# Kernel optimization log

Hardware: AMD Instinct MI355X
Metric: run time of the kernel (lower is better)

Reference implementation:

```python
import jax, jax.numpy as jnp
import numpy as np

N = 100000       # nodes
E = 3200000      # edges (before self loops)
EMB = 16         # embedding dim (EMB_SIZE)
H = 32           # hidden_size
NUM_EMB = 141
EDGE_DIM = 1     # NUM_EDGE_FEATURES
NEG_SLOPE = 0.2  # PyG GATConv default negative_slope


def setup_inputs() -> dict:
    key = jax.random.key(0)
    ks = jax.random.split(key, 18)
    f32 = jnp.float32
    return {
        "x_idx": jax.random.randint(ks[0], (N, 1), 0, NUM_EMB),
        "edge_index": jax.random.randint(ks[1], (2, E), 0, N),
        "edge_attr": jax.random.normal(ks[2], (E, EDGE_DIM), f32),
        # learned params
        "emb": jax.random.normal(ks[3], (NUM_EMB, EMB), f32) * 0.1,
        # conv1 (GATConv 16->32, heads=1, edge_dim=1)
        "W1": jax.random.normal(ks[4], (EMB, H), f32) * (1.0 / np.sqrt(EMB)),
        "as1": jax.random.normal(ks[5], (H,), f32) * 0.1,
        "ad1": jax.random.normal(ks[6], (H,), f32) * 0.1,
        "We1": jax.random.normal(ks[7], (EDGE_DIM, H), f32),
        "ae1": jax.random.normal(ks[8], (H,), f32) * 0.1,
        "b1": jnp.zeros((H,), f32),
        # conv2 (GATConv 32->32)
        "W2": jax.random.normal(ks[9], (H, H), f32) * (1.0 / np.sqrt(H)),
        "as2": jax.random.normal(ks[10], (H,), f32) * 0.1,
        "ad2": jax.random.normal(ks[11], (H,), f32) * 0.1,
        "We2": jax.random.normal(ks[12], (EDGE_DIM, H), f32),
        "ae2": jax.random.normal(ks[13], (H,), f32) * 0.1,
        "b2": jnp.zeros((H,), f32),
        # linear head 32->1
        "Wl": jax.random.normal(ks[14], (H, 1), f32) * (1.0 / np.sqrt(H)),
        "bl": jnp.zeros((1,), f32),
    }


def _add_self_loops(src, dst, ea):
    # PyG add_self_loops with fill_value='mean': loop edge_attr is the
    # segment-mean of incoming edge_attr per destination node.
    sums = jax.ops.segment_sum(ea, dst, num_segments=N)            # [N, EDGE_DIM]
    cnts = jax.ops.segment_sum(jnp.ones((ea.shape[0],), ea.dtype), dst, num_segments=N)
    loop_attr = sums / jnp.maximum(cnts, 1.0)[:, None]
    loop = jnp.arange(N, dtype=src.dtype)
    return (jnp.concatenate([src, loop]),
            jnp.concatenate([dst, loop]),
            jnp.concatenate([ea, loop_attr], axis=0))


def _gat_conv(x, src, dst, ea, W, a_s, a_d, We, a_e, b):
    h = x @ W                                   # [N, H]
    e = ea @ We                                 # [E2, H]
    alpha = jax.nn.leaky_relu((h @ a_s)[src] + (h @ a_d)[dst] + e @ a_e, NEG_SLOPE)
    # segment softmax over incoming edges of each dst node
    amax = jax.ops.segment_max(alpha, dst, num_segments=N)
    ex = jnp.exp(alpha - amax[dst])
    denom = jax.ops.segment_sum(ex, dst, num_segments=N)
    coef = ex / (denom[dst] + 1e-16)            # [E2]
    out = jax.ops.segment_sum(h[src] * coef[:, None], dst, num_segments=N)
    return out + b


def reference(x_idx, edge_index, edge_attr, emb, W1, as1, ad1, We1, ae1, b1,
              W2, as2, ad2, We2, ae2, b2, Wl, bl):
    src, dst, ea = _add_self_loops(edge_index[0], edge_index[1], edge_attr)
    x = emb[x_idx[:, 0]]                        # [N, EMB]
    x = _gat_conv(x, src, dst, ea, W1, as1, ad1, We1, ae1, b1)
    x = jax.nn.relu(x)                          # dropout is identity in eval mode
    x = _gat_conv(x, src, dst, ea, W2, as2, ad2, We2, ae2, b2)
    return x @ Wl + bl                          # [N, 1]
```

## Files before the change

### kernel.cpp

```cpp
#include <hip/hip_runtime.h>
#include <utility>

#define NN 100000
#define NE 3200000
#define H 32
#define EMBD 16
#define NEMB 141
#define NEG_SLOPE 0.2f
#define CSH 7
#define CN 128
#define NCO 782
#define CAP 4608
#define LCAP 4608
#define KCH 12800
#define GA 250

__device__ __forceinline__ float bf2f(unsigned short u) {
    return __int_as_float((int)u << 16);
}

template<class F, int... Is>
__device__ __forceinline__ void static_for_impl(F f, std::integer_sequence<int, Is...>) {
    (f(std::integral_constant<int, Is>{}), ...);
}
template<int N, class F>
__device__ __forceinline__ void static_for(F f) {
    static_for_impl(f, std::make_integer_sequence<int, N>{});
}

__global__ void k_tab(const float* __restrict__ emb, const float* __restrict__ W1,
                      const float* __restrict__ as1, const float* __restrict__ ad1,
                      const float* We1, const float* ae1,
                      const float* We2, const float* ae2,
                      const float* W2, const float* as2, const float* ad2,
                      const float* Wl, const float* b2, const float* bl,
                      float* tabH, float* tabS, float* tabD, float* scal,
                      float* was2, float* wad2, float* wl2, float* c0,
                      int* bcnt) {
    int gid = blockIdx.x * 64 + threadIdx.x;
    if (gid < NCO) bcnt[gid] = 0;
    int r = blockIdx.x, j = threadIdx.x;
    if (j >= 32) {
        if (r == 0 && j == 32) {
            float c1 = 0.f, c2 = 0.f;
            for (int k = 0; k < H; k++) {
                c1 += We1[k] * ae1[k];
                c2 += We2[k] * ae2[k];
            }
            scal[0] = c1; scal[1] = c2;
        }
        if (r == 1) {
            int k = j - 32;
            float s = 0.f, d = 0.f, l = 0.f;
            for (int q = 0; q < H; q++) {
                float w = W2[k * H + q];
                s += w * as2[q];
                d += w * ad2[q];
                l += w * Wl[q];
            }
            was2[k] = s; wad2[k] = d; wl2[k] = l;
        }
        if (r == 2 && j == 32) {
            float c = bl[0];
            for (int q = 0; q < H; q++) c += b2[q] * Wl[q];
            c0[0] = c;
        }
        return;
    }
    float acc = 0.f;
    #pragma unroll
    for (int k = 0; k < EMBD; k++) acc += emb[r * EMBD + k] * W1[k * H + j];
    tabH[r * H + j] = acc;
    float s = acc * as1[j];
    float d = acc * ad1[j];
    #pragma unroll
    for (int off = 16; off > 0; off >>= 1) {
        s += __shfl_down(s, off, 32);
        d += __shfl_down(d, off, 32);
    }
    if (j == 0) { tabS[r] = s; tabD[r] = d; }
}

__global__ __launch_bounds__(1024) void k_pscat(
                        const int* __restrict__ src, const int* __restrict__ dst,
                        const float* __restrict__ ea, const int* __restrict__ x_idx,
                        int* bcnt, long long* epk) {
    __shared__ long long st[KCH];
    __shared__ unsigned short cbuk[KCH];
    __shared__ int hist[NCO];
    __shared__ int scanb[1024];
    __shared__ int bas[NCO];
    __shared__ int allow[NCO];
    int t = threadIdx.x;
    int e0 = blockIdx.x * KCH;
    const int4*   d4 = (const int4*)(dst + e0);
    const int4*   s4 = (const int4*)(src + e0);
    const float4* a4 = (const float4*)(ea + e0);
    if (t < NCO) hist[t] = 0;
    __syncthreads();

    long long pkr[4][4];
    int       pcr[4][4];
    #pragma unroll
    for (int g = 0; g < 4; g++) {
        bool v = (g < 3) || (t < 128);
        if (v) {
            int gi = g * 1024 + t;
            int4 d = d4[gi];
            int4 s = s4[gi];
            float4 a = a4[gi];
            int x0 = x_idx[s.x], x1 = x_idx[s.y], x2 = x_idx[s.z], x3 = x_idx[s.w];
            int c0 = d.x >> CSH, c1 = d.y >> CSH, c2 = d.z >> CSH, c3 = d.w >> CSH;
            pkr[g][0] = ((long long)(unsigned)__float_as_int(a.x) << 32)
                      | (unsigned)(s.x | ((d.x & (CN - 1)) << 17) | (x0 << 24));
            pkr[g][1] = ((long long)(unsigned)__float_as_int(a.y) << 32)
                      | (unsigned)(s.y | ((d.y & (CN - 1)) << 17) | (x1 << 24));
            pkr[g][2] = ((long long)(unsigned)__float_as_int(a.z) << 32)
                      | (unsigned)(s.z | ((d.z & (CN - 1)) << 17) | (x2 << 24));
            pkr[g][3] = ((long long)(unsigned)__float_as_int(a.w) << 32)
                      | (unsigned)(s.w | ((d.w & (CN - 1)) << 17) | (x3 << 24));
            pcr[g][0] = (c0 << 14) | atomicAdd(&hist[c0], 1);
            pcr[g][1] = (c1 << 14) | atomicAdd(&hist[c1], 1);
            pcr[g][2] = (c2 << 14) | atomicAdd(&hist[c2], 1);
            pcr[g][3] = (c3 << 14) | atomicAdd(&hist[c3], 1);
        }
    }
    __syncthreads();

    int hv = (t < NCO) ? hist[t] : 0;
    scanb[t] = hv;
    __syncthreads();
    for (int s = 1; s < 1024; s <<= 1) {
        int x = (t >= s) ? scanb[t - s] : 0;
        __syncthreads();
        scanb[t] += x;
        __syncthreads();
    }
    scanb[t] -= hv;
    if (t < NCO) {
        if (hv) {
            int b = atomicAdd(&bcnt[t], hv);
            bas[t]   = t * CAP + b;
            allow[t] = CAP - b;
        } else {
            bas[t] = t * CAP; allow[t] = 0;
        }
    }
    __syncthreads();

    #pragma unroll
    for (int g = 0; g < 4; g++) {
        bool v = (g < 3) || (t < 128);
        if (v) {
            #pragma unroll
            for (int e = 0; e < 4; e++) {
                int c = pcr[g][e] >> 14;
                int r = pcr[g][e] & 0x3fff;
                int pos = scanb[c] + r;
                st[pos] = pkr[g][e];
                cbuk[pos] = (unsigned short)c;
            }
        }
    }
    __syncthreads();

    for (int i = t; i < KCH; i += 1024) {
        int c = cbuk[i];
        int l = i - scanb[c];
        if (l < allow[c]) epk[bas[c] + l] = st[i];
    }
}

__global__ void k_psort(const int* __restrict__ bcnt, long long* epk, int2* nfo) {
    __shared__ long long st[LCAP];
    __shared__ unsigned short rnk[LCAP];
    __shared__ int hist[CN], lofs[CN];
    int c = blockIdx.x, t = threadIdx.x;
    int base = c * CAP;
    int cnt = bcnt[c];
    if (cnt > CAP) cnt = CAP;
    if (t < CN) hist[t] = 0;
    __syncthreads();
    for (int k = t; k < cnt; k += 512) {
        long long pk = epk[base + k];
        st[k] = pk;
        rnk[k] = (unsigned short)atomicAdd(&hist[((int)pk >> 17) & (CN - 1)], 1);
    }
    __syncthreads();
    if (t < CN) lofs[t] = hist[t];
    __syncthreads();
    for (int s = 1; s < CN; s <<= 1) {
        int x = (t >= s && t < CN) ? lofs[t - s] : 0;
        __syncthreads();
        if (t < CN) lofs[t] += x;
        __syncthreads();
    }
    if (t < CN) {
        int ex = lofs[t] - hist[t];
        lofs[t] = ex;
        int node = c * CN + t;
        if (node < NN) nfo[node] = make_int2(base + ex, hist[t]);
    }
    __syncthreads();
    for (int k = t; k < cnt; k += 512) {
        long long pk = st[k];
        int ln = ((int)pk >> 17) & (CN - 1);
        epk[base + lofs[ln] + rnk[k]] = pk;
    }
}

__global__ void k_agg1(const int2* __restrict__ nfo, const long long* __restrict__ epk,
                       const float* __restrict__ tabS, const float* __restrict__ tabD,
                       const float* __restrict__ scal,
                       const float* __restrict__ tabH,
                       const int* __restrict__ xi,
                       const float* __restrict__ bias,
                       const float* __restrict__ was2, const float* __restrict__ wad2,
                       const float* __restrict__ wl2,
                       float2* __restrict__ g2, float* __restrict__ hd2) {
    int ln   = threadIdx.x & 7;
    int node = (blockIdx.x * blockDim.x + threadIdx.x) >> 3;
    if (node >= NN) return;
    int2 fo = nfo[node];
    int beg = fo.x;
    int dg  = fo.y;
    int end = beg + dg;
    float sc = scal[0];
    int xin = xi[node];
    float hdi = tabD[xin];

    float suma = 0.f, denp = 0.f;
    float4 acc = make_float4(0.f, 0.f, 0.f, 0.f);
    int base = beg;
    for (; end - base > 16; base += 32) {
        int pw[4] = {0, 0, 0, 0};
        #pragma unroll
        for (int e = 0; e < 4; e++) {
            int kk = base + 4 * ln + e;
            if (kk < end) {
                long long pk = epk[kk];
                int lo = (int)pk;
                float a = __int_as_float((int)(pk >> 32));
                suma += a;
                float hsv = tabS[(lo >> 24) & 0xff];
                float al = hsv + hdi + sc * a;
                al = (al > 0.f) ? al : NEG_SLOPE * al;
                int eb = __float_as_int(__expf(al));
                pw[e] = ((eb + 0x80) & 0xffffff00) | ((lo >> 24) & 0xff);
                denp += __int_as_float(pw[e] & 0xffffff00);
            }
        }
        static_for<32>([&](auto tc) {
            constexpr int t = decltype(tc)::value;
            int p = __builtin_amdgcn_ds_swizzle(pw[t & 3], ((t >> 2) << 5) | 0x18);
            float ext = __int_as_float(p & 0xffffff00);
            const float4 hv = *(const float4*)(tabH + ((p & 0xff) << 5) + (ln << 2));
            acc.x += ext * hv.x;
            acc.y += ext * hv.y;
            acc.z += ext * hv.z;
            acc.w += ext * hv.w;
        });
    }
    if (base < end) {
        int pw[2] = {0, 0};
        #pragma unroll
        for (int e = 0; e < 2; e++) {
            int kk = base + 2 * ln + e;
            if (kk < end) {
                long long pk = epk[kk];
                int lo = (int)pk;
                float a = __int_as_float((int)(pk >> 32));
                suma += a;
                float hsv = tabS[(lo >> 24) & 0xff];
                float al = hsv + hdi + sc * a;
                al = (al > 0.f) ? al : NEG_SLOPE * al;
                int eb = __float_as_int(__expf(al));
                pw[e] = ((eb + 0x80) & 0xffffff00) | ((lo >> 24) & 0xff);
                denp += __int_as_float(pw[e] & 0xffffff00);
            }
        }
        static_for<16>([&](auto tc) {
            constexpr int t = decltype(tc)::value;
            int p = __builtin_amdgcn_ds_swizzle(pw[t & 1], ((t >> 1) << 5) | 0x18);
            float ext = __int_as_float(p & 0xffffff00);
            const float4 hv = *(const float4*)(tabH + ((p & 0xff) << 5) + (ln << 2));
            acc.x += ext * hv.x;
            acc.y += ext * hv.y;
            acc.z += ext * hv.z;
            acc.w += ext * hv.w;
        });
    }
    #pragma unroll
    for (int o = 4; o > 0; o >>= 1) {
        suma += __shfl_xor(suma, o, 8);
        denp += __shfl_xor(denp, o, 8);
    }
    float la = suma / (float)((dg > 0) ? dg : 1);
    float alself = tabS[xin] + hdi + sc * la;
    alself = (alself > 0.f) ? alself : NEG_SLOPE * alself;
    float exs = __expf(alself);
    const float4 hvs = *(const float4*)(tabH + (xin << 5) + (ln << 2));
    acc.x += exs * hvs.x;
    acc.y += exs * hvs.y;
    acc.z += exs * hvs.z;
    acc.w += exs * hvs.w;
    float den = denp + exs + 1e-16f;

    const float4 b4 = *(const float4*)(bias + (ln << 2));
    float4 x;
    x.x = fmaxf(acc.x / den + b4.x, 0.f);
    x.y = fmaxf(acc.y / den + b4.y, 0.f);
    x.z = fmaxf(acc.z / den + b4.z, 0.f);
    x.w = fmaxf(acc.w / den + b4.w, 0.f);
    const float4 wa = *(const float4*)(was2 + (ln << 2));
    const float4 wd = *(const float4*)(wad2 + (ln << 2));
    const float4 wy = *(const float4*)(wl2  + (ln << 2));
    float sp = x.x * wa.x + x.y * wa.y + x.z * wa.z + x.w * wa.w;
    float dp = x.x * wd.x + x.y * wd.y + x.z * wd.z + x.w * wd.w;
    float yp = x.x * wy.x + x.y * wy.y + x.z * wy.z + x.w * wy.w;
    #pragma unroll
    for (int o = 4; o > 0; o >>= 1) {
        sp += __shfl_xor(sp, o, 8);
        dp += __shfl_xor(dp, o, 8);
        yp += __shfl_xor(yp, o, 8);
    }
    if (ln == 0) { g2[node] = make_float2(sp, yp); hd2[node] = dp; }
}

__global__ void k_agg2(const int2* __restrict__ nfo, const long long* __restrict__ epk,
                       const float2* __restrict__ g2, const float* __restrict__ hd2,
                       const float* __restrict__ scal, const float* __restrict__ c0p,
                       float* __restrict__ outF) {
    int lane = threadIdx.x & 31;
    int node = (blockIdx.x * blockDim.x + threadIdx.x) >> 5;
    if (node >= NN) return;
    int2 fo = nfo[node];
    int beg = fo.x;
    int dg  = fo.y;
    int end = beg + dg;
    float sc = scal[1];
    float hdi = hd2[node];
    float2 gn = g2[node];

    float num = 0.f, den = 0.f, suma = 0.f;
    for (int base = beg; base < end; base += 32) {
        int kk = base + lane;
        if (kk < end) {
            long long pk = epk[kk];
            float a = __int_as_float((int)(pk >> 32));
            int s = (int)pk & 0x1ffff;
            float2 g = g2[s];
            suma += a;
            float al = g.x + hdi + sc * a;
            al = (al > 0.f) ? al : NEG_SLOPE * al;
            float ex = __expf(al);
            num += ex * g.y;
            den += ex;
        }
    }
    #pragma unroll
    for (int o = 16; o > 0; o >>= 1) {
        num  += __shfl_xor(num, o, 32);
        den  += __shfl_xor(den, o, 32);
        suma += __shfl_xor(suma, o, 32);
    }
    float la = suma / (float)((dg > 0) ? dg : 1);
    float als = gn.x + hdi + sc * la;
    als = (als > 0.f) ? als : NEG_SLOPE * als;
    float exs = __expf(als);
    num += exs * gn.y;
    den += exs + 1e-16f;
    if (lane == 0) outF[node] = num / den + c0p[0];
}

extern "C" void kernel_launch(void* const* d_in, const int* in_sizes, int n_in,
                              void* d_out, int out_size, void* d_ws, size_t ws_size,
                              hipStream_t stream) {
    const int*   x_idx = (const int*)d_in[0];
    const int*   src   = (const int*)d_in[1];
    const int*   dst   = src + NE;
    const float* ea    = (const float*)d_in[2];
    const float* emb = (const float*)d_in[3];
    const float* W1  = (const float*)d_in[4];
    const float* as1 = (const float*)d_in[5];
    const float* ad1 = (const float*)d_in[6];
    const float* We1 = (const float*)d_in[7];
    const float* ae1 = (const float*)d_in[8];
    const float* b1  = (const float*)d_in[9];
    const float* W2  = (const float*)d_in[10];
    const float* as2 = (const float*)d_in[11];
    const float* ad2 = (const float*)d_in[12];
    const float* We2 = (const float*)d_in[13];
    const float* ae2 = (const float*)d_in[14];
    const float* b2  = (const float*)d_in[15];
    const float* Wl  = (const float*)d_in[16];
    const float* bl  = (const float*)d_in[17];
    float* out = (float*)d_out;

    float* ws   = (float*)d_ws;
    float* scal = ws;
    float* tabS = ws + 8;
    float* tabD = ws + 256;
    float* tabH = ws + 512;
    int*   bcnt = (int*)(ws + 5120);
    float* was2 = ws + 6144;
    float* wad2 = ws + 6208;
    float* wl2  = ws + 6272;
    float* c0   = ws + 6336;
    int2*  nfo = (int2*)(ws + 208192);
    float2* g2 = (float2*)(ws + 408192);
    long long* epk = (long long*)(ws + 2008192);
    float* hd2 = ws + 9315104;

    const int B = 256;
    int g1 = (NN * 8 + B - 1) / B;
    int g2g = (NN * H + B - 1) / B;

    k_tab<<<NEMB, 64, 0, stream>>>(emb, W1, as1, ad1, We1, ae1, We2, ae2,
                                   W2, as2, ad2, Wl, b2, bl,
                                   tabH, tabS, tabD, scal,
                                   was2, wad2, wl2, c0, bcnt);
    k_pscat<<<GA, 1024, 0, stream>>>(src, dst, ea, x_idx, bcnt, epk);
    k_psort<<<NCO, 512, 0, stream>>>(bcnt, epk, nfo);
    k_agg1<<<g1, B, 0, stream>>>(nfo, epk, tabS, tabD, scal, tabH,
                                 x_idx, b1, was2, wad2, wl2, g2, hd2);
    k_agg2<<<g2g, B, 0, stream>>>(nfo, epk, g2, hd2, scal, c0, out);
}
```

Baseline: 214.8 us.

## Fuse per-chunk node sort into both aggregation kernels via shared memory

```diff
diff --git a/kernel.cpp b/kernel.cpp
--- a/kernel.cpp
+++ b/kernel.cpp
@@ -14,10 +14,6 @@
 #define LCAP 4608
 #define KCH 12800
 #define GA 250
-
-__device__ __forceinline__ float bf2f(unsigned short u) {
-    return __int_as_float((int)u << 16);
-}
 
 template<class F, int... Is>
 __device__ __forceinline__ void static_for_impl(F f, std::integer_sequence<int, Is...>) {
@@ -171,45 +167,8 @@
     }
 }
 
-__global__ void k_psort(const int* __restrict__ bcnt, long long* epk, int2* nfo) {
-    __shared__ long long st[LCAP];
-    __shared__ unsigned short rnk[LCAP];
-    __shared__ int hist[CN], lofs[CN];
-    int c = blockIdx.x, t = threadIdx.x;
-    int base = c * CAP;
-    int cnt = bcnt[c];
-    if (cnt > CAP) cnt = CAP;
-    if (t < CN) hist[t] = 0;
-    __syncthreads();
-    for (int k = t; k < cnt; k += 512) {
-        long long pk = epk[base + k];
-        st[k] = pk;
-        rnk[k] = (unsigned short)atomicAdd(&hist[((int)pk >> 17) & (CN - 1)], 1);
-    }
-    __syncthreads();
-    if (t < CN) lofs[t] = hist[t];
-    __syncthreads();
-    for (int s = 1; s < CN; s <<= 1) {
-        int x = (t >= s && t < CN) ? lofs[t - s] : 0;
-        __syncthreads();
-        if (t < CN) lofs[t] += x;
-        __syncthreads();
-    }
-    if (t < CN) {
-        int ex = lofs[t] - hist[t];
-        lofs[t] = ex;
-        int node = c * CN + t;
-        if (node < NN) nfo[node] = make_int2(base + ex, hist[t]);
-    }
-    __syncthreads();
-    for (int k = t; k < cnt; k += 512) {
-        long long pk = st[k];
-        int ln = ((int)pk >> 17) & (CN - 1);
-        epk[base + lofs[ln] + rnk[k]] = pk;
-    }
-}
-
-__global__ void k_agg1(const int2* __restrict__ nfo, const long long* __restrict__ epk,
+__global__ __launch_bounds__(1024) void k_bagg1(
+                       const int* __restrict__ bcnt, const long long* __restrict__ epk,
                        const float* __restrict__ tabS, const float* __restrict__ tabD,
                        const float* __restrict__ scal,
                        const float* __restrict__ tabH,
@@ -218,12 +177,47 @@
                        const float* __restrict__ was2, const float* __restrict__ wad2,
                        const float* __restrict__ wl2,
                        float2* __restrict__ g2, float* __restrict__ hd2) {
-    int ln   = threadIdx.x & 7;
-    int node = (blockIdx.x * blockDim.x + threadIdx.x) >> 3;
+    __shared__ long long st[LCAP];
+    __shared__ int hist[CN], lofs[CN];
+    int c = blockIdx.x, t = threadIdx.x;
+    int wbase = c * CAP;
+    int cnt = bcnt[c];
+    if (cnt > CAP) cnt = CAP;
+    if (t < CN) hist[t] = 0;
+    __syncthreads();
+
+    long long pk0 = 0, pk1 = 0, pk2 = 0, pk3 = 0, pk4 = 0;
+    int rk0 = 0, rk1 = 0, rk2 = 0, rk3 = 0, rk4 = 0;
+    #define LDRK(J) { int k = (J) * 1024 + t; if (k < cnt) { \
+        pk##J = epk[wbase + k]; \
+        rk##J = atomicAdd(&hist[((int)pk##J >> 17) & (CN - 1)], 1); } }
+    LDRK(0) LDRK(1) LDRK(2) LDRK(3) LDRK(4)
+    #undef LDRK
+    __syncthreads();
+
+    if (t < CN) lofs[t] = hist[t];
+    __syncthreads();
+    for (int s = 1; s < CN; s <<= 1) {
+        int x = (t >= s && t < CN) ? lofs[t - s] : 0;
+        __syncthreads();
+        if (t < CN) lofs[t] += x;
+        __syncthreads();
+    }
+    if (t < CN) lofs[t] -= hist[t];
+    __syncthreads();
+
+    #define SCT(J) { int k = (J) * 1024 + t; if (k < cnt) \
+        st[lofs[((int)pk##J >> 17) & (CN - 1)] + rk##J] = pk##J; }
+    SCT(0) SCT(1) SCT(2) SCT(3) SCT(4)
+    #undef SCT
+    __syncthreads();
+
+    int ln   = t & 7;
+    int nl   = t >> 3;
+    int node = c * CN + nl;
     if (node >= NN) return;
-    int2 fo = nfo[node];
-    int beg = fo.x;
-    int dg  = fo.y;
+    int beg = lofs[nl];
+    int dg  = hist[nl];
     int end = beg + dg;
     float sc = scal[0];
     int xin = xi[node];
@@ -231,14 +225,14 @@
 
     float suma = 0.f, denp = 0.f;
     float4 acc = make_float4(0.f, 0.f, 0.f, 0.f);
-    int base = beg;
-    for (; end - base > 16; base += 32) {
+    int bse = beg;
+    for (; end - bse > 16; bse += 32) {
         int pw[4] = {0, 0, 0, 0};
         #pragma unroll
         for (int e = 0; e < 4; e++) {
-            int kk = base + 4 * ln + e;
+            int kk = bse + 4 * ln + e;
             if (kk < end) {
-                long long pk = epk[kk];
+                long long pk = st[kk];
                 int lo = (int)pk;
                 float a = __int_as_float((int)(pk >> 32));
                 suma += a;
@@ -251,8 +245,8 @@
             }
         }
         static_for<32>([&](auto tc) {
-            constexpr int t = decltype(tc)::value;
-            int p = __builtin_amdgcn_ds_swizzle(pw[t & 3], ((t >> 2) << 5) | 0x18);
+            constexpr int tt = decltype(tc)::value;
+            int p = __builtin_amdgcn_ds_swizzle(pw[tt & 3], ((tt >> 2) << 5) | 0x18);
             float ext = __int_as_float(p & 0xffffff00);
             const float4 hv = *(const float4*)(tabH + ((p & 0xff) << 5) + (ln << 2));
             acc.x += ext * hv.x;
@@ -261,13 +255,13 @@
             acc.w += ext * hv.w;
         });
     }
-    if (base < end) {
+    if (bse < end) {
         int pw[2] = {0, 0};
         #pragma unroll
         for (int e = 0; e < 2; e++) {
-            int kk = base + 2 * ln + e;
+            int kk = bse + 2 * ln + e;
             if (kk < end) {
-                long long pk = epk[kk];
+                long long pk = st[kk];
                 int lo = (int)pk;
                 float a = __int_as_float((int)(pk >> 32));
                 suma += a;
@@ -280,8 +274,8 @@
             }
         }
         static_for<16>([&](auto tc) {
-            constexpr int t = decltype(tc)::value;
-            int p = __builtin_amdgcn_ds_swizzle(pw[t & 1], ((t >> 1) << 5) | 0x18);
+            constexpr int tt = decltype(tc)::value;
+            int p = __builtin_amdgcn_ds_swizzle(pw[tt & 1], ((tt >> 1) << 5) | 0x18);
             float ext = __int_as_float(p & 0xffffff00);
             const float4 hv = *(const float4*)(tabH + ((p & 0xff) << 5) + (ln << 2));
             acc.x += ext * hv.x;
@@ -327,42 +321,75 @@
     if (ln == 0) { g2[node] = make_float2(sp, yp); hd2[node] = dp; }
 }
 
-__global__ void k_agg2(const int2* __restrict__ nfo, const long long* __restrict__ epk,
+__global__ __launch_bounds__(1024) void k_bagg2(
+                       const int* __restrict__ bcnt, const long long* __restrict__ epk,
                        const float2* __restrict__ g2, const float* __restrict__ hd2,
                        const float* __restrict__ scal, const float* __restrict__ c0p,
                        float* __restrict__ outF) {
-    int lane = threadIdx.x & 31;
-    int node = (blockIdx.x * blockDim.x + threadIdx.x) >> 5;
+    __shared__ long long st[LCAP];
+    __shared__ int hist[CN], lofs[CN];
+    int c = blockIdx.x, t = threadIdx.x;
+    int wbase = c * CAP;
+    int cnt = bcnt[c];
+    if (cnt > CAP) cnt = CAP;
+    if (t < CN) hist[t] = 0;
+    __syncthreads();
+
+    long long pk0 = 0, pk1 = 0, pk2 = 0, pk3 = 0, pk4 = 0;
+    int rk0 = 0, rk1 = 0, rk2 = 0, rk3 = 0, rk4 = 0;
+    #define LDRK(J) { int k = (J) * 1024 + t; if (k < cnt) { \
+        pk##J = epk[wbase + k]; \
+        rk##J = atomicAdd(&hist[((int)pk##J >> 17) & (CN - 1)], 1); } }
+    LDRK(0) LDRK(1) LDRK(2) LDRK(3) LDRK(4)
+    #undef LDRK
+    __syncthreads();
+
+    if (t < CN) lofs[t] = hist[t];
+    __syncthreads();
+    for (int s = 1; s < CN; s <<= 1) {
+        int x = (t >= s && t < CN) ? lofs[t - s] : 0;
+        __syncthreads();
+        if (t < CN) lofs[t] += x;
+        __syncthreads();
+    }
+    if (t < CN) lofs[t] -= hist[t];
+    __syncthreads();
+
+    #define SCT(J) { int k = (J) * 1024 + t; if (k < cnt) \
+        st[lofs[((int)pk##J >> 17) & (CN - 1)] + rk##J] = pk##J; }
+    SCT(0) SCT(1) SCT(2) SCT(3) SCT(4)
+    #undef SCT
+    __syncthreads();
+
+    int ln   = t & 7;
+    int nl   = t >> 3;
+    int node = c * CN + nl;
     if (node >= NN) return;
-    int2 fo = nfo[node];
-    int beg = fo.x;
-    int dg  = fo.y;
+    int beg = lofs[nl];
+    int dg  = hist[nl];
     int end = beg + dg;
     float sc = scal[1];
     float hdi = hd2[node];
     float2 gn = g2[node];
 
     float num = 0.f, den = 0.f, suma = 0.f;
-    for (int base = beg; base < end; base += 32) {
-        int kk = base + lane;
-        if (kk < end) {
-            long long pk = epk[kk];
-            float a = __int_as_float((int)(pk >> 32));
-            int s = (int)pk & 0x1ffff;
-            float2 g = g2[s];
-            suma += a;
-            float al = g.x + hdi + sc * a;
-            al = (al > 0.f) ? al : NEG_SLOPE * al;
-            float ex = __expf(al);
-            num += ex * g.y;
-            den += ex;
-        }
-    }
-    #pragma unroll
-    for (int o = 16; o > 0; o >>= 1) {
-        num  += __shfl_xor(num, o, 32);
-        den  += __shfl_xor(den, o, 32);
-        suma += __shfl_xor(suma, o, 32);
+    for (int kk = beg + ln; kk < end; kk += 8) {
+        long long pk = st[kk];
+        float a = __int_as_float((int)(pk >> 32));
+        int s = (int)pk & 0x1ffff;
+        float2 g = g2[s];
+        suma += a;
+        float al = g.x + hdi + sc * a;
+        al = (al > 0.f) ? al : NEG_SLOPE * al;
+        float ex = __expf(al);
+        num += ex * g.y;
+        den += ex;
+    }
+    #pragma unroll
+    for (int o = 4; o > 0; o >>= 1) {
+        num  += __shfl_xor(num, o, 8);
+        den  += __shfl_xor(den, o, 8);
+        suma += __shfl_xor(suma, o, 8);
     }
     float la = suma / (float)((dg > 0) ? dg : 1);
     float als = gn.x + hdi + sc * la;
@@ -370,7 +397,7 @@
     float exs = __expf(als);
     num += exs * gn.y;
     den += exs + 1e-16f;
-    if (lane == 0) outF[node] = num / den + c0p[0];
+    if (ln == 0) outF[node] = num / den + c0p[0];
 }
 
 extern "C" void kernel_launch(void* const* d_in, const int* in_sizes, int n_in,
@@ -407,22 +434,16 @@
     float* wad2 = ws + 6208;
     float* wl2  = ws + 6272;
     float* c0   = ws + 6336;
-    int2*  nfo = (int2*)(ws + 208192);
     float2* g2 = (float2*)(ws + 408192);
     long long* epk = (long long*)(ws + 2008192);
     float* hd2 = ws + 9315104;
-
-    const int B = 256;
-    int g1 = (NN * 8 + B - 1) / B;
-    int g2g = (NN * H + B - 1) / B;
 
     k_tab<<<NEMB, 64, 0, stream>>>(emb, W1, as1, ad1, We1, ae1, We2, ae2,
                                    W2, as2, ad2, Wl, b2, bl,
                                    tabH, tabS, tabD, scal,
                                    was2, wad2, wl2, c0, bcnt);
     k_pscat<<<GA, 1024, 0, stream>>>(src, dst, ea, x_idx, bcnt, epk);
-    k_psort<<<NCO, 512, 0, stream>>>(bcnt, epk, nfo);
-    k_agg1<<<g1, B, 0, stream>>>(nfo, epk, tabS, tabD, scal, tabH,
-                                 x_idx, b1, was2, wad2, wl2, g2, hd2);
-    k_agg2<<<g2g, B, 0, stream>>>(nfo, epk, g2, hd2, scal, c0, out);
-}
+    k_bagg1<<<NCO, 1024, 0, stream>>>(bcnt, epk, tabS, tabD, scal, tabH,
+                                      x_idx, b1, was2, wad2, wl2, g2, hd2);
+    k_bagg2<<<NCO, 1024, 0, stream>>>(bcnt, epk, g2, hd2, scal, c0, out);
+}
```

Measured after the change: 203.9 us. 1.05x faster.

## Fuse per-bucket sort into layer-1 aggregation and shrink scatter chunks

Applied to the files above, without the earlier changes.

```diff
diff --git a/kernel.cpp b/kernel.cpp
--- a/kernel.cpp
+++ b/kernel.cpp
@@ -12,12 +12,8 @@
 #define NCO 782
 #define CAP 4608
 #define LCAP 4608
-#define KCH 12800
-#define GA 250
-
-__device__ __forceinline__ float bf2f(unsigned short u) {
-    return __int_as_float((int)u << 16);
-}
+#define KCH 6400
+#define GA 500
 
 template<class F, int... Is>
 __device__ __forceinline__ void static_for_impl(F f, std::integer_sequence<int, Is...>) {
@@ -88,9 +84,10 @@
     __shared__ long long st[KCH];
     __shared__ unsigned short cbuk[KCH];
     __shared__ int hist[NCO];
-    __shared__ int scanb[1024];
+    __shared__ int scanb[NCO];
     __shared__ int bas[NCO];
     __shared__ int allow[NCO];
+    __shared__ int wsum[16], woff[16];
     int t = threadIdx.x;
     int e0 = blockIdx.x * KCH;
     const int4*   d4 = (const int4*)(dst + e0);
@@ -99,11 +96,11 @@
     if (t < NCO) hist[t] = 0;
     __syncthreads();
 
-    long long pkr[4][4];
-    int       pcr[4][4];
-    #pragma unroll
-    for (int g = 0; g < 4; g++) {
-        bool v = (g < 3) || (t < 128);
+    long long pkr[2][4];
+    int       pcr[2][4];
+    #pragma unroll
+    for (int g = 0; g < 2; g++) {
+        bool v = (g < 1) || (t < 576);
         if (v) {
             int gi = g * 1024 + t;
             int4 d = d4[gi];
@@ -127,19 +124,30 @@
     }
     __syncthreads();
 
-    int hv = (t < NCO) ? hist[t] : 0;
-    scanb[t] = hv;
-    __syncthreads();
-    for (int s = 1; s < 1024; s <<= 1) {
-        int x = (t >= s) ? scanb[t - s] : 0;
-        __syncthreads();
-        scanb[t] += x;
-        __syncthreads();
-    }
-    scanb[t] -= hv;
+    int v = (t < NCO) ? hist[t] : 0;
+    int inc = v;
+    #pragma unroll
+    for (int o = 1; o < 64; o <<= 1) {
+        int x = __shfl_up(inc, o, 64);
+        if ((t & 63) >= o) inc += x;
+    }
+    if ((t & 63) == 63) wsum[t >> 6] = inc;
+    __syncthreads();
+    if (t < 16) {
+        int wv = wsum[t];
+        int winc = wv;
+        #pragma unroll
+        for (int o = 1; o < 16; o <<= 1) {
+            int x = __shfl_up(winc, o, 16);
+            if (t >= o) winc += x;
+        }
+        woff[t] = winc - wv;
+    }
+    __syncthreads();
+    if (t < NCO) scanb[t] = inc - v + woff[t >> 6];
     if (t < NCO) {
-        if (hv) {
-            int b = atomicAdd(&bcnt[t], hv);
+        if (v) {
+            int b = atomicAdd(&bcnt[t], v);
             bas[t]   = t * CAP + b;
             allow[t] = CAP - b;
         } else {
@@ -149,9 +157,9 @@
     __syncthreads();
 
     #pragma unroll
-    for (int g = 0; g < 4; g++) {
-        bool v = (g < 3) || (t < 128);
-        if (v) {
+    for (int g = 0; g < 2; g++) {
+        bool vv = (g < 1) || (t < 576);
+        if (vv) {
             #pragma unroll
             for (int e = 0; e < 4; e++) {
                 int c = pcr[g][e] >> 14;
@@ -171,45 +179,8 @@
     }
 }
 
-__global__ void k_psort(const int* __restrict__ bcnt, long long* epk, int2* nfo) {
-    __shared__ long long st[LCAP];
-    __shared__ unsigned short rnk[LCAP];
-    __shared__ int hist[CN], lofs[CN];
-    int c = blockIdx.x, t = threadIdx.x;
-    int base = c * CAP;
-    int cnt = bcnt[c];
-    if (cnt > CAP) cnt = CAP;
-    if (t < CN) hist[t] = 0;
-    __syncthreads();
-    for (int k = t; k < cnt; k += 512) {
-        long long pk = epk[base + k];
-        st[k] = pk;
-        rnk[k] = (unsigned short)atomicAdd(&hist[((int)pk >> 17) & (CN - 1)], 1);
-    }
-    __syncthreads();
-    if (t < CN) lofs[t] = hist[t];
-    __syncthreads();
-    for (int s = 1; s < CN; s <<= 1) {
-        int x = (t >= s && t < CN) ? lofs[t - s] : 0;
-        __syncthreads();
-        if (t < CN) lofs[t] += x;
-        __syncthreads();
-    }
-    if (t < CN) {
-        int ex = lofs[t] - hist[t];
-        lofs[t] = ex;
-        int node = c * CN + t;
-        if (node < NN) nfo[node] = make_int2(base + ex, hist[t]);
-    }
-    __syncthreads();
-    for (int k = t; k < cnt; k += 512) {
-        long long pk = st[k];
-        int ln = ((int)pk >> 17) & (CN - 1);
-        epk[base + lofs[ln] + rnk[k]] = pk;
-    }
-}
-
-__global__ void k_agg1(const int2* __restrict__ nfo, const long long* __restrict__ epk,
+__global__ __launch_bounds__(1024) void k_bagg1(
+                       const int* __restrict__ bcnt, long long* __restrict__ epk,
                        const float* __restrict__ tabS, const float* __restrict__ tabD,
                        const float* __restrict__ scal,
                        const float* __restrict__ tabH,
@@ -217,13 +188,59 @@
                        const float* __restrict__ bias,
                        const float* __restrict__ was2, const float* __restrict__ wad2,
                        const float* __restrict__ wl2,
-                       float2* __restrict__ g2, float* __restrict__ hd2) {
-    int ln   = threadIdx.x & 7;
-    int node = (blockIdx.x * blockDim.x + threadIdx.x) >> 3;
+                       float2* __restrict__ g2, float* __restrict__ hd2,
+                       int2* __restrict__ nfo) {
+    __shared__ long long st[LCAP];
+    __shared__ int hist[CN], lofs[CN];
+    int c = blockIdx.x, t = threadIdx.x;
+    int wbase = c * CAP;
+    int cnt = bcnt[c];
+    if (cnt > CAP) cnt = CAP;
+    if (t < CN) hist[t] = 0;
+    __syncthreads();
+
+    long long pk0 = 0, pk1 = 0, pk2 = 0, pk3 = 0, pk4 = 0;
+    int rk0 = 0, rk1 = 0, rk2 = 0, rk3 = 0, rk4 = 0;
+    #define LDRK(J) { int k = (J) * 1024 + t; if (k < cnt) { \
+        pk##J = epk[wbase + k]; \
+        rk##J = atomicAdd(&hist[((int)pk##J >> 17) & (CN - 1)], 1); } }
+    LDRK(0) LDRK(1) LDRK(2) LDRK(3) LDRK(4)
+    #undef LDRK
+    __syncthreads();
+
+    if (t < 64) {
+        int v0 = hist[2 * t], v1 = hist[2 * t + 1];
+        int s = v0 + v1;
+        int inc = s;
+        #pragma unroll
+        for (int o = 1; o < 64; o <<= 1) {
+            int x = __shfl_up(inc, o, 64);
+            if (t >= o) inc += x;
+        }
+        int ex = inc - s;
+        lofs[2 * t] = ex;
+        lofs[2 * t + 1] = ex + v0;
+    }
+    __syncthreads();
+
+    #define SCT(J) { int k = (J) * 1024 + t; if (k < cnt) \
+        st[lofs[((int)pk##J >> 17) & (CN - 1)] + rk##J] = pk##J; }
+    SCT(0) SCT(1) SCT(2) SCT(3) SCT(4)
+    #undef SCT
+    __syncthreads();
+
+    for (int i = t; i < cnt; i += 1024) epk[wbase + i] = st[i];
+    if (t < CN) {
+        int node = c * CN + t;
+        if (node < NN) nfo[node] = make_int2(wbase + lofs[t], hist[t]);
+    }
+
+    int ln   = t & 7;
+    int nl   = t >> 3;
+    int node = c * CN + nl;
     if (node >= NN) return;
-    int2 fo = nfo[node];
-    int beg = fo.x;
-    int dg  = fo.y;
+    int beg = lofs[nl];
+    int dg  = hist[nl];
     int end = beg + dg;
     float sc = scal[0];
     int xin = xi[node];
@@ -231,14 +248,14 @@
 
     float suma = 0.f, denp = 0.f;
     float4 acc = make_float4(0.f, 0.f, 0.f, 0.f);
-    int base = beg;
-    for (; end - base > 16; base += 32) {
+    int bse = beg;
+    for (; end - bse > 16; bse += 32) {
         int pw[4] = {0, 0, 0, 0};
         #pragma unroll
         for (int e = 0; e < 4; e++) {
-            int kk = base + 4 * ln + e;
+            int kk = bse + 4 * ln + e;
             if (kk < end) {
-                long long pk = epk[kk];
+                long long pk = st[kk];
                 int lo = (int)pk;
                 float a = __int_as_float((int)(pk >> 32));
                 suma += a;
@@ -251,8 +268,8 @@
             }
         }
         static_for<32>([&](auto tc) {
-            constexpr int t = decltype(tc)::value;
-            int p = __builtin_amdgcn_ds_swizzle(pw[t & 3], ((t >> 2) << 5) | 0x18);
+            constexpr int tt = decltype(tc)::value;
+            int p = __builtin_amdgcn_ds_swizzle(pw[tt & 3], ((tt >> 2) << 5) | 0x18);
             float ext = __int_as_float(p & 0xffffff00);
             const float4 hv = *(const float4*)(tabH + ((p & 0xff) << 5) + (ln << 2));
             acc.x += ext * hv.x;
@@ -261,13 +278,13 @@
             acc.w += ext * hv.w;
         });
     }
-    if (base < end) {
+    if (bse < end) {
         int pw[2] = {0, 0};
         #pragma unroll
         for (int e = 0; e < 2; e++) {
-            int kk = base + 2 * ln + e;
+            int kk = bse + 2 * ln + e;
             if (kk < end) {
-                long long pk = epk[kk];
+                long long pk = st[kk];
                 int lo = (int)pk;
                 float a = __int_as_float((int)(pk >> 32));
                 suma += a;
@@ -280,8 +297,8 @@
             }
         }
         static_for<16>([&](auto tc) {
-            constexpr int t = decltype(tc)::value;
-            int p = __builtin_amdgcn_ds_swizzle(pw[t & 1], ((t >> 1) << 5) | 0x18);
+            constexpr int tt = decltype(tc)::value;
+            int p = __builtin_amdgcn_ds_swizzle(pw[tt & 1], ((tt >> 1) << 5) | 0x18);
             float ext = __int_as_float(p & 0xffffff00);
             const float4 hv = *(const float4*)(tabH + ((p & 0xff) << 5) + (ln << 2));
             acc.x += ext * hv.x;
@@ -413,7 +430,6 @@
     float* hd2 = ws + 9315104;
 
     const int B = 256;
-    int g1 = (NN * 8 + B - 1) / B;
     int g2g = (NN * H + B - 1) / B;
 
     k_tab<<<NEMB, 64, 0, stream>>>(emb, W1, as1, ad1, We1, ae1, We2, ae2,
@@ -421,8 +437,7 @@
                                    tabH, tabS, tabD, scal,
                                    was2, wad2, wl2, c0, bcnt);
     k_pscat<<<GA, 1024, 0, stream>>>(src, dst, ea, x_idx, bcnt, epk);
-    k_psort<<<NCO, 512, 0, stream>>>(bcnt, epk, nfo);
-    k_agg1<<<g1, B, 0, stream>>>(nfo, epk, tabS, tabD, scal, tabH,
-                                 x_idx, b1, was2, wad2, wl2, g2, hd2);
+    k_bagg1<<<NCO, 1024, 0, stream>>>(bcnt, epk, tabS, tabD, scal, tabH,
+                                      x_idx, b1, was2, wad2, wl2, g2, hd2, nfo);
     k_agg2<<<g2g, B, 0, stream>>>(nfo, epk, g2, hd2, scal, c0, out);
 }
```

Result: faster. 208.1 us (-3.1%).
